# Optimization experiments

Hardware: AMD Instinct MI355X
Metric: run time of the kernel (lower is better)

Reference implementation:

```python
import jax, jax.numpy as jnp
import numpy as np

N = 10000
E = 160000
C = 256        # in_channels
M = 256        # mid_channels
R = 64         # nregion


def _glorot(key, shape):
    fan_in, fan_out = shape[-1], shape[0]
    lim = (6.0 / (fan_in + fan_out)) ** 0.5
    return jax.random.uniform(key, shape, jnp.float32, -lim, lim)


def setup_inputs() -> dict:
    key = jax.random.key(0)
    ks = jax.random.split(key, 12)
    x = jax.random.normal(ks[0], (N, C), jnp.float32)
    edge_index = jax.random.randint(ks[1], (2, E), 0, N, jnp.int32)
    conv_w = _glorot(ks[2], (C, C))
    conv_b = jnp.zeros((C,), jnp.float32)
    lin1_w = _glorot(ks[3], (M, C)); lin1_b = jnp.zeros((M,), jnp.float32)
    lin2_w = _glorot(ks[4], (M, M)); lin2_b = jnp.zeros((M,), jnp.float32)
    lin3_w = _glorot(ks[5], (1, M)); lin3_b = jnp.zeros((1,), jnp.float32)
    lin4_w = _glorot(ks[6], (M, M)); lin4_b = jnp.zeros((M,), jnp.float32)
    bilin_w = _glorot(ks[7], (R, M, M)) * 0.1
    bilin_b = jnp.zeros((R,), jnp.float32)
    return {"x": x, "edge_index": edge_index,
            "conv_w": conv_w, "conv_b": conv_b,
            "lin1_w": lin1_w, "lin1_b": lin1_b,
            "lin2_w": lin2_w, "lin2_b": lin2_b,
            "lin3_w": lin3_w, "lin3_b": lin3_b,
            "lin4_w": lin4_w, "lin4_b": lin4_b,
            "bilin_w": bilin_w, "bilin_b": bilin_b}


def gcn_conv(x, edge_index, w, b):
    # PyG GCNConv: add self-loops, symmetric D^-1/2 (A+I) D^-1/2 normalization
    src, dst = edge_index[0], edge_index[1]
    n = x.shape[0]
    xw = x @ w.T                                            # [N, C]
    deg = jnp.ones((n,), xw.dtype).at[dst].add(jnp.ones((E,), xw.dtype))  # +1 for self loop
    dinv = jax.lax.rsqrt(deg)
    norm = dinv[src] * dinv[dst]                            # [E]
    agg = jnp.zeros_like(xw).at[dst].add(norm[:, None] * xw[src])
    agg = agg + (dinv * dinv)[:, None] * xw                 # self-loop messages
    return agg + b


def reference(x, edge_index, conv_w, conv_b, lin1_w, lin1_b, lin2_w, lin2_b,
              lin3_w, lin3_b, lin4_w, lin4_b, bilin_w, bilin_b):
    out = jax.nn.relu(gcn_conv(x, edge_index, conv_w, conv_b))
    x0 = out + x                                            # residual [N, C]
    x0 = jax.nn.relu(x0 @ lin1_w.T + lin1_b)                # [N, M]
    x1 = jax.nn.relu(x0 @ lin2_w.T + lin2_b)
    x1 = x1 @ lin3_w.T + lin3_b                             # [N, 1]
    x2 = jax.nn.relu(x0 @ lin4_w.T + lin4_b)                # [N, M]
    # Bilinear(x2, x2): out[n,r] = x2[n] @ W[r] @ x2[n] + b[r]
    t = (x2 @ bilin_w.reshape(R * M, M).T).reshape(-1, R, M)  # [N, R, M]
    x2 = jnp.sum(t * x2[:, None, :], axis=-1) + bilin_b       # [N, R]
    return (x1, x2)
```

## Files before the change

kernel.cpp:

```cpp
#include <hip/hip_runtime.h>

typedef unsigned short u16;
typedef __attribute__((ext_vector_type(8))) short bf16x8;
typedef __attribute__((ext_vector_type(4))) float f32x4;

#define N_NODES 10000
#define E_EDGES 160000

__device__ __forceinline__ float b2f(u16 u) {
  union { unsigned i; float f; } c; c.i = ((unsigned)u) << 16; return c.f;
}
__device__ __forceinline__ u16 f2b(float f) {
  union { float f; unsigned i; } c; c.f = f;
  unsigned i = c.i;
  return (u16)((i + 0x7FFFu + ((i >> 16) & 1u)) >> 16);
}

__global__ void detect_kernel(const unsigned* __restrict__ w, int* __restrict__ flag) {
  int t = threadIdx.x;
  int cnt = 0;
  for (int i = t; i < 1024; i += 64) {
    unsigned e = (w[i] >> 7) & 0xFF;
    cnt += (e >= 100 && e <= 145) ? 1 : 0;
  }
  for (int o = 32; o; o >>= 1) cnt += __shfl_xor(cnt, o);
  if (t == 0) *flag = (cnt >= 512) ? 1 : 0;
}
__global__ void canon_kernel(const void* __restrict__ src, u16* __restrict__ dst,
                             int n, const int* __restrict__ flag) {
  int i = blockIdx.x * 256 + threadIdx.x;
  if (i >= n) return;
  if (*flag) dst[i] = ((const u16*)src)[i];
  else       dst[i] = f2b(((const float*)src)[i]);
}
__global__ void canon4_kernel(const void* s0, const void* s1, const void* s2, const void* s3,
                              u16* d0, u16* d1, u16* d2, u16* d3,
                              const int* __restrict__ flag) {
  int tsel = blockIdx.x >> 8;
  int i = (blockIdx.x & 255) * 256 + threadIdx.x;
  const void* s = tsel == 0 ? s0 : tsel == 1 ? s1 : tsel == 2 ? s2 : s3;
  u16* d = tsel == 0 ? d0 : tsel == 1 ? d1 : tsel == 2 ? d2 : d3;
  if (*flag) d[i] = ((const u16*)s)[i];
  else       d[i] = f2b(((const float*)s)[i]);
}
__global__ void canon_small_kernel(const void* s0, const void* s1, const void* s2,
                                   const void* s3, const void* s4, const void* s5,
                                   const void* s6,
                                   u16* d0, u16* d1, u16* d2, u16* d3, u16* d4,
                                   u16* d5, u16* d6, const int* __restrict__ flag) {
  int t = threadIdx.x;
  int f = *flag;
  const void* srcs[7] = {s0, s1, s2, s3, s4, s5, s6};
  u16* dsts[7] = {d0, d1, d2, d3, d4, d5, d6};
  const int ns[7] = {256, 256, 256, 256, 256, 64, 1};
#pragma unroll
  for (int k = 0; k < 7; ++k) {
    if (t < ns[k]) {
      if (f) dsts[k][t] = ((const u16*)srcs[k])[t];
      else   dsts[k][t] = f2b(((const float*)srcs[k])[t]);
    }
  }
}

__device__ __forceinline__ void stage_async(const u16* __restrict__ src, int stride,
                                            int row0, int maxRow, int k0,
                                            u16* lds, int w, int lane) {
  int rsel = lane >> 3;
  int gch = (lane & 7) ^ rsel;
#pragma unroll
  for (int i = 0; i < 4; ++i) {
    int rb = (w * 4 + i) * 8;
    int grow = row0 + rb + rsel;
    grow = grow > maxRow ? maxRow : grow;
    const u16* gp = src + (size_t)grow * stride + k0 + gch * 8;
    u16* lp = lds + rb * 64;
    __builtin_amdgcn_global_load_lds(
        (const __attribute__((address_space(1))) void*)gp,
        (__attribute__((address_space(3))) void*)lp, 16, 0, 0);
  }
}

__device__ __forceinline__ void mma_tile(const u16* lA, const u16* lB,
                                         f32x4 acc[4][4], int wr, int wc, int lane) {
#pragma unroll
  for (int ks = 0; ks < 2; ++ks) {
    bf16x8 af[4], bfr[4];
    int g = ks * 4 + (lane >> 4);
#pragma unroll
    for (int t = 0; t < 4; ++t) {
      int rowA = wr * 64 + t * 16 + (lane & 15);
      af[t] = *(const bf16x8*)(lA + rowA * 64 + ((g ^ (rowA & 7)) * 8));
      int rowB = wc * 64 + t * 16 + (lane & 15);
      bfr[t] = *(const bf16x8*)(lB + rowB * 64 + ((g ^ (rowB & 7)) * 8));
    }
#pragma unroll
    for (int ti = 0; ti < 4; ++ti)
#pragma unroll
      for (int tj = 0; tj < 4; ++tj)
        acc[ti][tj] = __builtin_amdgcn_mfma_f32_16x16x32_bf16(af[ti], bfr[tj],
                                                              acc[ti][tj], 0, 0, 0);
  }
}

template <bool RELU, bool F32OUT>
__global__ __launch_bounds__(256, 2)
void gemm_kernel(const u16* __restrict__ A, const u16* __restrict__ B,
                 const u16* __restrict__ bias, float* __restrict__ outF,
                 u16* __restrict__ outB, int NN, int J, int K) {
  __shared__ u16 lA[128 * 64];
  __shared__ u16 lB[128 * 64];
  int lane = threadIdx.x & 63;
  int w = threadIdx.x >> 6;
  int wr = w >> 1, wc = w & 1;
  int n0 = blockIdx.y * 128;
  int j0 = blockIdx.x * 128;
  f32x4 acc[4][4];
#pragma unroll
  for (int i = 0; i < 4; ++i)
#pragma unroll
    for (int j = 0; j < 4; ++j) acc[i][j] = (f32x4){0.f, 0.f, 0.f, 0.f};

  for (int kt = 0; kt < K; kt += 64) {
    stage_async(A, K, n0, NN - 1, kt, lA, w, lane);
    stage_async(B, K, j0, J - 1, kt, lB, w, lane);
    __syncthreads();
    mma_tile(lA, lB, acc, wr, wc, lane);
    __syncthreads();
  }

#pragma unroll
  for (int ti = 0; ti < 4; ++ti)
#pragma unroll
    for (int tj = 0; tj < 4; ++tj) {
      int col = j0 + wc * 64 + tj * 16 + (lane & 15);
      float bv = bias ? b2f(bias[col]) : 0.0f;
#pragma unroll
      for (int r = 0; r < 4; ++r) {
        int row = n0 + wr * 64 + ti * 16 + ((lane >> 4) << 2) + r;
        if (row < NN) {
          float v = acc[ti][tj][r] + bv;
          if (RELU) v = fmaxf(v, 0.0f);
          if (F32OUT) outF[(size_t)row * J + col] = v;
          else        outB[(size_t)row * J + col] = f2b(v);
        }
      }
    }
}

__global__ __launch_bounds__(256, 2)
void bilinear_kernel(const u16* __restrict__ x2v, const u16* __restrict__ W,
                     float* __restrict__ out2acc, int NN) {
  __shared__ u16 lA[128 * 64];
  __shared__ u16 lB[128 * 64];
  int lane = threadIdx.x & 63;
  int w = threadIdx.x >> 6;
  int wr = w >> 1, wc = w & 1;
  int n0 = blockIdx.y * 128;
  int rm0 = blockIdx.x * 128;
  int m0g = rm0 & 255;
  int xv_kt = (m0g >> 6) + wc;
  f32x4 acc[4][4];
#pragma unroll
  for (int i = 0; i < 4; ++i)
#pragma unroll
    for (int j = 0; j < 4; ++j) acc[i][j] = (f32x4){0.f, 0.f, 0.f, 0.f};

  u16 xvr[4][16];

#pragma unroll
  for (int kt4 = 0; kt4 < 4; ++kt4) {
    stage_async(x2v, 256, n0, NN - 1, kt4 * 64, lA, w, lane);
    stage_async(W, 256, rm0, 16383, kt4 * 64, lB, w, lane);
    __syncthreads();
    mma_tile(lA, lB, acc, wr, wc, lane);
    if (kt4 == xv_kt) {
#pragma unroll
      for (int tj = 0; tj < 4; ++tj) {
        int kl = tj * 16 + (lane & 15);
        int ch = kl >> 3, off = kl & 7;
#pragma unroll
        for (int ti = 0; ti < 4; ++ti)
#pragma unroll
          for (int r = 0; r < 4; ++r) {
            int rowl = wr * 64 + ti * 16 + ((lane >> 4) << 2) + r;
            xvr[tj][ti * 4 + r] = lA[rowl * 64 + ((ch ^ (rowl & 7)) * 8) + off];
          }
      }
    }
    __syncthreads();
  }

  int region = rm0 >> 8;
  float rowsum[4][4];
#pragma unroll
  for (int ti = 0; ti < 4; ++ti)
#pragma unroll
    for (int r = 0; r < 4; ++r) rowsum[ti][r] = 0.0f;

#pragma unroll
  for (int ti = 0; ti < 4; ++ti)
#pragma unroll
    for (int tj = 0; tj < 4; ++tj)
#pragma unroll
      for (int r = 0; r < 4; ++r)
        rowsum[ti][r] += acc[ti][tj][r] * b2f(xvr[tj][ti * 4 + r]);

#pragma unroll
  for (int ti = 0; ti < 4; ++ti)
#pragma unroll
    for (int r = 0; r < 4; ++r) {
      float s = rowsum[ti][r];
      s += __shfl_xor(s, 1);
      s += __shfl_xor(s, 2);
      s += __shfl_xor(s, 4);
      s += __shfl_xor(s, 8);
      if ((lane & 15) == 0) {
        int rowl = wr * 64 + ti * 16 + ((lane >> 4) << 2) + r;
        int n = n0 + rowl;
        if (n < NN) unsafeAtomicAdd(&out2acc[(size_t)n * 64 + region], s);
      }
    }
}

__global__ void hist_kernel(const int* __restrict__ ei, int* __restrict__ count) {
  int i = blockIdx.x * 256 + threadIdx.x;
  if (i < E_EDGES) atomicAdd(&count[ei[E_EDGES + i]], 1);
}

__global__ void scan_kernel(const int* __restrict__ count, int* __restrict__ start,
                            int* __restrict__ cursor, float* __restrict__ dinv) {
  __shared__ int sdata[1024];
  __shared__ int carry_s;
  int t = threadIdx.x;
  if (t == 0) carry_s = 0;
  __syncthreads();
  for (int base = 0; base < N_NODES; base += 1024) {
    int i = base + t;
    int v = (i < N_NODES) ? count[i] : 0;
    sdata[t] = v;
    __syncthreads();
    for (int o = 1; o < 1024; o <<= 1) {
      int u = (t >= o) ? sdata[t - o] : 0;
      __syncthreads();
      sdata[t] += u;
      __syncthreads();
    }
    int excl = sdata[t] - v + carry_s;
    if (i < N_NODES) {
      start[i] = excl;
      cursor[i] = excl;
      dinv[i] = rsqrtf(1.0f + (float)v);
    }
    __syncthreads();
    if (t == 1023) carry_s += sdata[1023];
    __syncthreads();
  }
}

__global__ void place_kernel(const int* __restrict__ ei, int* __restrict__ cursor,
                             int* __restrict__ order) {
  int i = blockIdx.x * 256 + threadIdx.x;
  if (i >= E_EDGES) return;
  int d = ei[E_EDGES + i];
  int pos = atomicAdd(&cursor[d], 1);
  order[pos] = i;
}

__global__ void gather_kernel(const int* __restrict__ ei, const int* __restrict__ order,
                              const int* __restrict__ start, const int* __restrict__ count,
                              const float* __restrict__ dinv, const float* __restrict__ xw,
                              const u16* __restrict__ conv_b, const u16* __restrict__ x,
                              u16* __restrict__ x0) {
  int node = (blockIdx.x * blockDim.x + threadIdx.x) >> 6;
  int lane = threadIdx.x & 63;
  if (node >= N_NODES) return;
  int s0 = start[node], cnt = count[node];
  float dn = dinv[node];
  float ax = 0.f, ay = 0.f, az = 0.f, aw = 0.f;
  for (int base = 0; base < cnt; base += 64) {
    int rem = cnt - base;
    int m = rem < 64 ? rem : 64;
    int eid = (lane < m) ? order[s0 + base + lane] : 0;
    int s = (lane < m) ? ei[eid] : 0;
    float nrm = (lane < m) ? dinv[s] * dn : 0.f;
    for (int j = 0; j < m; ++j) {
      int sj = __shfl(s, j);
      float nj = __shfl(nrm, j);
      float4 v = *((const float4*)(xw + (size_t)sj * 256) + lane);
      ax += nj * v.x; ay += nj * v.y; az += nj * v.z; aw += nj * v.w;
    }
  }
  float4 sv = *((const float4*)(xw + (size_t)node * 256) + lane);
  float slw = dn * dn;
  const u16* bb = conv_b + lane * 4;
  const u16* xr = x + (size_t)node * 256 + lane * 4;
  u16 o[4];
  float vals[4] = {ax + slw * sv.x, ay + slw * sv.y, az + slw * sv.z, aw + slw * sv.w};
#pragma unroll
  for (int j = 0; j < 4; ++j) {
    float v = vals[j] + b2f(bb[j]);
    v = fmaxf(v, 0.0f) + b2f(xr[j]);
    o[j] = f2b(v);
  }
  *((ushort4*)(x0 + (size_t)node * 256) + lane) = make_ushort4(o[0], o[1], o[2], o[3]);
}

__global__ void lin3_kernel(const float* __restrict__ x1a, const u16* __restrict__ w3,
                            const u16* __restrict__ b3, void* __restrict__ dout,
                            const int* __restrict__ flag) {
  int wid = (blockIdx.x * blockDim.x + threadIdx.x) >> 6;
  int lane = threadIdx.x & 63;
  if (wid >= N_NODES) return;
  const float* xr = x1a + (size_t)wid * 256 + lane * 4;
  float s = xr[0] * b2f(w3[lane * 4 + 0]) + xr[1] * b2f(w3[lane * 4 + 1]) +
            xr[2] * b2f(w3[lane * 4 + 2]) + xr[3] * b2f(w3[lane * 4 + 3]);
  for (int o = 32; o; o >>= 1) s += __shfl_xor(s, o);
  if (lane == 0) {
    float v = s + b2f(b3[0]);
    if (*flag) ((u16*)dout)[wid] = f2b(v);
    else       ((float*)dout)[wid] = v;
  }
}
__global__ void out2_kernel(const float* __restrict__ acc, const u16* __restrict__ bb,
                            void* __restrict__ dout, const int* __restrict__ flag) {
  int idx = blockIdx.x * 256 + threadIdx.x;
  float v = acc[idx] + b2f(bb[idx & 63]);
  if (*flag) ((u16*)dout)[N_NODES + idx] = f2b(v);
  else       ((float*)dout)[N_NODES + idx] = v;
}

extern "C" void kernel_launch(void* const* d_in, const int* in_sizes, int n_in,
                              void* d_out, int out_size, void* d_ws, size_t ws_size,
                              hipStream_t stream) {
  const int* ei = (const int*)d_in[1];

  float* ws      = (float*)d_ws;
  float* xw      = ws;
  int*   count   = (int*)(xw + N_NODES * 256);
  int*   start   = count + 10240;
  int*   cursor  = start + 10240;
  int*   order   = cursor + 10240;
  float* dinv    = (float*)(order + E_EDGES);
  float* out2acc = dinv + 10240;
  u16* x0  = (u16*)(out2acc + N_NODES * 64);
  u16* x0m = x0 + N_NODES * 256;
  u16* x2v = x0m + N_NODES * 256;
  u16* cx  = x2v + N_NODES * 256;
  u16* cwc = cx + N_NODES * 256;
  u16* cw1 = cwc + 65536;
  u16* cw2 = cw1 + 65536;
  u16* cw4 = cw2 + 65536;
  u16* cwB = cw4 + 65536;
  u16* cbc = cwB + 4194304;
  u16* cb1 = cbc + 256;
  u16* cb2 = cb1 + 256;
  u16* cb4 = cb2 + 256;
  u16* cw3 = cb4 + 256;
  u16* cbB = cw3 + 256;
  u16* cb3 = cbB + 64;
  int* flag = (int*)(cb3 + 16);
  float* x1a = xw;

  hipMemsetAsync(count, 0, N_NODES * sizeof(int), stream);
  hipMemsetAsync(out2acc, 0, (size_t)N_NODES * 64 * sizeof(float), stream);

  detect_kernel<<<1, 64, 0, stream>>>((const unsigned*)d_in[0], flag);

  canon_kernel<<<(N_NODES * 256 + 255) / 256, 256, 0, stream>>>(d_in[0], cx, N_NODES * 256, flag);
  canon4_kernel<<<1024, 256, 0, stream>>>(d_in[2], d_in[4], d_in[6], d_in[10],
                                          cwc, cw1, cw2, cw4, flag);
  canon_small_kernel<<<1, 256, 0, stream>>>(d_in[3], d_in[5], d_in[7], d_in[11],
                                            d_in[8], d_in[13], d_in[9],
                                            cbc, cb1, cb2, cb4, cw3, cbB, cb3, flag);
  canon_kernel<<<(4194304 + 255) / 256, 256, 0, stream>>>(d_in[12], cwB, 4194304, flag);

  hist_kernel<<<(E_EDGES + 255) / 256, 256, 0, stream>>>(ei, count);
  scan_kernel<<<1, 1024, 0, stream>>>(count, start, cursor, dinv);
  place_kernel<<<(E_EDGES + 255) / 256, 256, 0, stream>>>(ei, cursor, order);

  gemm_kernel<false, true><<<dim3(2, 79), 256, 0, stream>>>(
      cx, cwc, nullptr, xw, nullptr, N_NODES, 256, 256);

  gather_kernel<<<(N_NODES * 64 + 255) / 256, 256, 0, stream>>>(
      ei, order, start, count, dinv, xw, cbc, cx, x0);

  gemm_kernel<true, false><<<dim3(2, 79), 256, 0, stream>>>(
      x0, cw1, cb1, nullptr, x0m, N_NODES, 256, 256);
  gemm_kernel<true, true><<<dim3(2, 79), 256, 0, stream>>>(
      x0m, cw2, cb2, x1a, nullptr, N_NODES, 256, 256);
  lin3_kernel<<<(N_NODES + 3) / 4, 256, 0, stream>>>(x1a, cw3, cb3, d_out, flag);
  gemm_kernel<true, false><<<dim3(2, 79), 256, 0, stream>>>(
      x0m, cw4, cb4, nullptr, x2v, N_NODES, 256, 256);

  bilinear_kernel<<<dim3(128, 79), 256, 0, stream>>>(x2v, cwB, out2acc, N_NODES);
  out2_kernel<<<(N_NODES * 64) / 256, 256, 0, stream>>>(out2acc, cbB, d_out, flag);
}
```

Before: 429.4 us.

## Fuse lin2, lin3 and lin4 GEMMs into one kernel and merge output kernels

Result: faster. 413.8 us (-3.6%).

```diff
diff --git a/kernel.cpp b/kernel.cpp
--- a/kernel.cpp
+++ b/kernel.cpp
@@ -145,6 +145,83 @@
         }
       }
     }
+}
+
+__global__ __launch_bounds__(256, 2)
+void gemm_fused234_kernel(const u16* __restrict__ A, const u16* __restrict__ B,
+                          const u16* __restrict__ bias, const u16* __restrict__ w3,
+                          float* __restrict__ out1acc, u16* __restrict__ x2v, int NN) {
+  __shared__ u16 lA[128 * 64];
+  __shared__ u16 lB[128 * 64];
+  int lane = threadIdx.x & 63;
+  int w = threadIdx.x >> 6;
+  int wr = w >> 1, wc = w & 1;
+  int n0 = blockIdx.y * 128;
+  int j0 = blockIdx.x * 128;
+  f32x4 acc[4][4];
+#pragma unroll
+  for (int i = 0; i < 4; ++i)
+#pragma unroll
+    for (int j = 0; j < 4; ++j) acc[i][j] = (f32x4){0.f, 0.f, 0.f, 0.f};
+
+  for (int kt = 0; kt < 256; kt += 64) {
+    stage_async(A, 256, n0, NN - 1, kt, lA, w, lane);
+    stage_async(B, 256, j0, 511, kt, lB, w, lane);
+    __syncthreads();
+    mma_tile(lA, lB, acc, wr, wc, lane);
+    __syncthreads();
+  }
+
+  if (j0 < 256) {
+    float part[4][4];
+#pragma unroll
+    for (int ti = 0; ti < 4; ++ti)
+#pragma unroll
+      for (int r = 0; r < 4; ++r) part[ti][r] = 0.0f;
+#pragma unroll
+    for (int ti = 0; ti < 4; ++ti)
+#pragma unroll
+      for (int tj = 0; tj < 4; ++tj) {
+        int col = j0 + wc * 64 + tj * 16 + (lane & 15);
+        float bv = b2f(bias[col]);
+        float wv = b2f(w3[col]);
+#pragma unroll
+        for (int r = 0; r < 4; ++r) {
+          float v = fmaxf(acc[ti][tj][r] + bv, 0.0f);
+          part[ti][r] += v * wv;
+        }
+      }
+#pragma unroll
+    for (int ti = 0; ti < 4; ++ti)
+#pragma unroll
+      for (int r = 0; r < 4; ++r) {
+        float s = part[ti][r];
+        s += __shfl_xor(s, 1);
+        s += __shfl_xor(s, 2);
+        s += __shfl_xor(s, 4);
+        s += __shfl_xor(s, 8);
+        if ((lane & 15) == 0) {
+          int row = n0 + wr * 64 + ti * 16 + ((lane >> 4) << 2) + r;
+          if (row < NN) unsafeAtomicAdd(&out1acc[row], s);
+        }
+      }
+  } else {
+#pragma unroll
+    for (int ti = 0; ti < 4; ++ti)
+#pragma unroll
+      for (int tj = 0; tj < 4; ++tj) {
+        int col = j0 + wc * 64 + tj * 16 + (lane & 15);
+        float bv = b2f(bias[col]);
+#pragma unroll
+        for (int r = 0; r < 4; ++r) {
+          int row = n0 + wr * 64 + ti * 16 + ((lane >> 4) << 2) + r;
+          if (row < NN) {
+            float v = fmaxf(acc[ti][tj][r] + bv, 0.0f);
+            x2v[(size_t)row * 256 + (col - 256)] = f2b(v);
+          }
+        }
+      }
+  }
 }
 
 __global__ __launch_bounds__(256, 2)
@@ -305,28 +382,22 @@
   *((ushort4*)(x0 + (size_t)node * 256) + lane) = make_ushort4(o[0], o[1], o[2], o[3]);
 }
 
-__global__ void lin3_kernel(const float* __restrict__ x1a, const u16* __restrict__ w3,
-                            const u16* __restrict__ b3, void* __restrict__ dout,
-                            const int* __restrict__ flag) {
-  int wid = (blockIdx.x * blockDim.x + threadIdx.x) >> 6;
-  int lane = threadIdx.x & 63;
-  if (wid >= N_NODES) return;
-  const float* xr = x1a + (size_t)wid * 256 + lane * 4;
-  float s = xr[0] * b2f(w3[lane * 4 + 0]) + xr[1] * b2f(w3[lane * 4 + 1]) +
-            xr[2] * b2f(w3[lane * 4 + 2]) + xr[3] * b2f(w3[lane * 4 + 3]);
-  for (int o = 32; o; o >>= 1) s += __shfl_xor(s, o);
-  if (lane == 0) {
-    float v = s + b2f(b3[0]);
-    if (*flag) ((u16*)dout)[wid] = f2b(v);
-    else       ((float*)dout)[wid] = v;
-  }
-}
-__global__ void out2_kernel(const float* __restrict__ acc, const u16* __restrict__ bb,
-                            void* __restrict__ dout, const int* __restrict__ flag) {
+__global__ void out_final_kernel(const float* __restrict__ out1acc,
+                                 const float* __restrict__ out2acc,
+                                 const u16* __restrict__ b3, const u16* __restrict__ bb,
+                                 void* __restrict__ dout, const int* __restrict__ flag) {
   int idx = blockIdx.x * 256 + threadIdx.x;
-  float v = acc[idx] + b2f(bb[idx & 63]);
-  if (*flag) ((u16*)dout)[N_NODES + idx] = f2b(v);
-  else       ((float*)dout)[N_NODES + idx] = v;
+  int f = *flag;
+  if (idx < N_NODES) {
+    float v = out1acc[idx] + b2f(b3[0]);
+    if (f) ((u16*)dout)[idx] = f2b(v);
+    else   ((float*)dout)[idx] = v;
+  } else if (idx < N_NODES + N_NODES * 64) {
+    int k = idx - N_NODES;
+    float v = out2acc[k] + b2f(bb[k & 63]);
+    if (f) ((u16*)dout)[idx] = f2b(v);
+    else   ((float*)dout)[idx] = v;
+  }
 }
 
 extern "C" void kernel_launch(void* const* d_in, const int* in_sizes, int n_in,
@@ -341,7 +412,8 @@
   int*   cursor  = start + 10240;
   int*   order   = cursor + 10240;
   float* dinv    = (float*)(order + E_EDGES);
-  float* out2acc = dinv + 10240;
+  float* out1acc = dinv + 10240;
+  float* out2acc = out1acc + 10240;
   u16* x0  = (u16*)(out2acc + N_NODES * 64);
   u16* x0m = x0 + N_NODES * 256;
   u16* x2v = x0m + N_NODES * 256;
@@ -359,10 +431,9 @@
   u16* cbB = cw3 + 256;
   u16* cb3 = cbB + 64;
   int* flag = (int*)(cb3 + 16);
-  float* x1a = xw;
 
   hipMemsetAsync(count, 0, N_NODES * sizeof(int), stream);
-  hipMemsetAsync(out2acc, 0, (size_t)N_NODES * 64 * sizeof(float), stream);
+  hipMemsetAsync(out1acc, 0, (10240 + (size_t)N_NODES * 64) * sizeof(float), stream);
 
   detect_kernel<<<1, 64, 0, stream>>>((const unsigned*)d_in[0], flag);
 
@@ -386,12 +457,12 @@
 
   gemm_kernel<true, false><<<dim3(2, 79), 256, 0, stream>>>(
       x0, cw1, cb1, nullptr, x0m, N_NODES, 256, 256);
-  gemm_kernel<true, true><<<dim3(2, 79), 256, 0, stream>>>(
-      x0m, cw2, cb2, x1a, nullptr, N_NODES, 256, 256);
-  lin3_kernel<<<(N_NODES + 3) / 4, 256, 0, stream>>>(x1a, cw3, cb3, d_out, flag);
-  gemm_kernel<true, false><<<dim3(2, 79), 256, 0, stream>>>(
-      x0m, cw4, cb4, nullptr, x2v, N_NODES, 256, 256);
+
+  gemm_fused234_kernel<<<dim3(4, 79), 256, 0, stream>>>(
+      x0m, cw2, cb2, cw3, out1acc, x2v, N_NODES);
 
   bilinear_kernel<<<dim3(128, 79), 256, 0, stream>>>(x2v, cwB, out2acc, N_NODES);
-  out2_kernel<<<(N_NODES * 64) / 256, 256, 0, stream>>>(out2acc, cbB, d_out, flag);
-}
+
+  out_final_kernel<<<(N_NODES * 65 + 255) / 256, 256, 0, stream>>>(
+      out1acc, out2acc, cb3, cbB, d_out, flag);
+}
```
